# Performance work log

Measured on AMD Instinct MI355X. Metric: run time of the kernel, lower is better.

## Reference

```python
import jax, jax.numpy as jnp
import numpy as np

FORGET_BIAS = 1.0

def _lstm_step(c, h, x, W, b):
    # TF BasicLSTMCell: concat([x, h]) @ W + b -> split into i, j, f, o
    gates = jnp.concatenate([x, h], axis=-1) @ W + b
    i, j, f, o = jnp.split(gates, 4, axis=-1)
    new_c = c * jax.nn.sigmoid(f + FORGET_BIAS) + jax.nn.sigmoid(i) * jnp.tanh(j)
    new_h = jnp.tanh(new_c) * jax.nn.sigmoid(o)
    return new_c, new_h

def setup_inputs() -> dict:
    key = jax.random.key(0)
    ks = jax.random.split(key, 8)
    B, T, D, H, C = 64, 128, 2048, 512, 101
    s1 = 1.0 / np.sqrt(D + H)
    s2 = 1.0 / np.sqrt(2 * H)
    so = 1.0 / np.sqrt(H)
    return {
        "inputs": jax.random.normal(ks[0], (B, T, D), dtype=jnp.float32),
        "labels": jax.random.randint(ks[1], (B, T), 0, C, dtype=jnp.int64),
        "W1": jax.random.normal(ks[2], (D + H, 4 * H), dtype=jnp.float32) * s1,
        "b1": jnp.zeros((4 * H,), dtype=jnp.float32),
        "W2": jax.random.normal(ks[3], (2 * H, 4 * H), dtype=jnp.float32) * s2,
        "b2": jnp.zeros((4 * H,), dtype=jnp.float32),
        "Wout": jax.random.normal(ks[4], (H, C), dtype=jnp.float32) * so,
        "bout": jnp.zeros((C,), dtype=jnp.float32),
    }

def reference(inputs, labels, W1, b1, W2, b2, Wout, bout):
    B, T, D = inputs.shape
    H = Wout.shape[0]

    def step(carry, x_t):
        (c1, h1), (c2, h2) = carry
        c1, h1 = _lstm_step(c1, h1, x_t, W1, b1)
        c2, h2 = _lstm_step(c2, h2, h1, W2, b2)
        return ((c1, h1), (c2, h2)), h2

    zeros = jnp.zeros((B, H), dtype=inputs.dtype)
    init = ((zeros, zeros), (zeros, zeros))
    xs = jnp.swapaxes(inputs, 0, 1)  # [T, B, D]
    _, hs = jax.lax.scan(step, init, xs)  # hs: [T, B, H]
    outputs = jnp.swapaxes(hs, 0, 1)  # [B, T, H]

    logits = outputs @ Wout + bout  # [B, T, C]
    preds = jax.nn.softmax(logits, axis=-1)
    log_probs = jax.nn.log_softmax(logits, axis=-1)
    ce = -jnp.take_along_axis(log_probs, labels[..., None], axis=-1)[..., 0]  # [B, T]
    cost = jnp.mean(jnp.sum(ce, axis=1))
    return preds, cost
```

## Files before the change

### kernel.cpp

```cpp
#include <hip/hip_runtime.h>
#include <cmath>

#define Bb   64
#define Tt   128
#define Dd   2048
#define Hh   512
#define Gg   2048
#define Cc   101
#define PC   112
#define ROWS 8192

typedef unsigned short u16;
typedef __attribute__((ext_vector_type(8))) short bf16x8;
typedef __attribute__((ext_vector_type(4))) float f32x4;

#define PAD32 40
#define PAD128 136

#define GLOAD_LDS16(g, l) __builtin_amdgcn_global_load_lds(                  \
    (const __attribute__((address_space(1))) unsigned int*)(const void*)(g), \
    (__attribute__((address_space(3))) unsigned int*)(void*)(l), 16, 0, 0)

__device__ __forceinline__ u16 bf16rne(float x) {
  unsigned u = __float_as_uint(x);
  unsigned r = (u + 0x7fffu + ((u >> 16) & 1u)) >> 16;
  return (u16)r;
}
__device__ __forceinline__ void split_bf16(float x, u16& h, u16& l) {
  h = bf16rne(x);
  l = bf16rne(x - __uint_as_float(((unsigned)h) << 16));
}
__device__ __forceinline__ float sigm(float x) { return 1.f / (1.f + expf(-x)); }

__global__ __launch_bounds__(256)
void convert_hilo(const float* __restrict__ src, u16* __restrict__ hi,
                  u16* __restrict__ lo, int n4) {
  for (int i = blockIdx.x * 256 + threadIdx.x; i < n4; i += gridDim.x * 256) {
    const float4 v = ((const float4*)src)[i];
    ushort4 h, l;
    split_bf16(v.x, h.x, l.x);
    split_bf16(v.y, h.y, l.y);
    split_bf16(v.z, h.z, l.z);
    split_bf16(v.w, h.w, l.w);
    ((ushort4*)hi)[i] = h;
    ((ushort4*)lo)[i] = l;
  }
}

__global__ __launch_bounds__(256)
void convertT_w1(const float* __restrict__ W1, u16* __restrict__ Th,
                 u16* __restrict__ Tl) {
  __shared__ float tl[32][33];
  const int tx = threadIdx.x, ty = threadIdx.y;
  const int k0 = blockIdx.x * 32, c0 = blockIdx.y * 32;
#pragma unroll
  for (int j = 0; j < 4; ++j)
    tl[ty + j * 8][tx] = W1[(size_t)(k0 + ty + j * 8) * Gg + (c0 + tx)];
  __syncthreads();
#pragma unroll
  for (int j = 0; j < 4; ++j) {
    const float v = tl[tx][ty + j * 8];
    u16 h, l;
    split_bf16(v, h, l);
    const size_t o = (size_t)(c0 + ty + j * 8) * Dd + (k0 + tx);
    Th[o] = h;
    Tl[o] = l;
  }
}

__global__ __launch_bounds__(256)
void convert_woutT(const float* __restrict__ Wout, u16* __restrict__ Th,
                   u16* __restrict__ Tl) {
  const int c = blockIdx.x;
  for (int k = threadIdx.x; k < Hh; k += 256) {
    const float v = (c < Cc) ? Wout[k * Cc + c] : 0.f;
    u16 h, l;
    split_bf16(v, h, l);
    Th[c * Hh + k] = h;
    Tl[c * Hh + k] = l;
  }
}

__global__ __launch_bounds__(256)
void permuteW(const float* __restrict__ src, u16* __restrict__ dh,
              u16* __restrict__ dl, int K) {
  __shared__ float tl[32][33];
  const int tx = threadIdx.x, ty = threadIdx.y;
  const int k0 = blockIdx.x * 32, c0 = blockIdx.y * 32;
#pragma unroll
  for (int j = 0; j < 4; ++j)
    tl[ty + j * 8][tx] = src[(size_t)(k0 + ty + j * 8) * Gg + (c0 + tx)];
  __syncthreads();
#pragma unroll
  for (int j = 0; j < 4; ++j) {
    const int col = c0 + ty + j * 8;
    const int g = col >> 9, mg = col & 511;
    const int cg = mg >> 2, m = mg & 3;
    const float v = tl[tx][ty + j * 8];
    u16 h, l;
    split_bf16(v, h, l);
    const size_t o = (size_t)(cg * 16 + g * 4 + m) * K + k0 + tx;
    dh[o] = h;
    dl[o] = l;
  }
}

__global__ __launch_bounds__(256)
void gemm1_mfma(const u16* __restrict__ Ah, const u16* __restrict__ Al,
                const u16* __restrict__ Bh, const u16* __restrict__ Bl,
                const float* __restrict__ bias, float* __restrict__ C) {
  __shared__ u16 Ash[128][32];
  __shared__ u16 Asl[128][32];
  __shared__ u16 Bsh[128][32];
  __shared__ u16 Bsl[128][32];
  const int tid  = threadIdx.x;
  const int lane = tid & 63, wave = tid >> 6;
  const int wm = wave >> 1, wn = wave & 1;
  const int l15 = lane & 15, q = lane >> 4, r4 = (lane >> 4) * 4;
  const int lin = blockIdx.x;
  const int xcd = lin & 7, s = lin >> 3;
  const int bx = 2 * xcd + (s & 1);
  const int by = s >> 1;
  const int row0 = by * 128, col0 = bx * 128;

  const int sr = tid >> 2, sc = (tid & 3) * 8;
  const u16* gA0h = Ah + (size_t)(row0 + sr) * Dd + sc;
  const u16* gA1h = Ah + (size_t)(row0 + 64 + sr) * Dd + sc;
  const u16* gA0l = Al + (size_t)(row0 + sr) * Dd + sc;
  const u16* gA1l = Al + (size_t)(row0 + 64 + sr) * Dd + sc;
  const u16* gB0h = Bh + (size_t)(col0 + sr) * Dd + sc;
  const u16* gB1h = Bh + (size_t)(col0 + 64 + sr) * Dd + sc;
  const u16* gB0l = Bl + (size_t)(col0 + sr) * Dd + sc;
  const u16* gB1l = Bl + (size_t)(col0 + 64 + sr) * Dd + sc;
  u16* lA0h = &Ash[sr][sc];      u16* lA1h = &Ash[64 + sr][sc];
  u16* lA0l = &Asl[sr][sc];      u16* lA1l = &Asl[64 + sr][sc];
  u16* lB0h = &Bsh[sr][sc];      u16* lB1h = &Bsh[64 + sr][sc];
  u16* lB0l = &Bsl[sr][sc];      u16* lB1l = &Bsl[64 + sr][sc];

  f32x4 acc[4][4];
#pragma unroll
  for (int i = 0; i < 4; ++i)
#pragma unroll
    for (int j = 0; j < 4; ++j) acc[i][j] = (f32x4){0.f, 0.f, 0.f, 0.f};

  for (int k0 = 0; k0 < Dd; k0 += 32) {
    GLOAD_LDS16(gA0h + k0, lA0h);
    GLOAD_LDS16(gA1h + k0, lA1h);
    GLOAD_LDS16(gA0l + k0, lA0l);
    GLOAD_LDS16(gA1l + k0, lA1l);
    GLOAD_LDS16(gB0h + k0, lB0h);
    GLOAD_LDS16(gB1h + k0, lB1h);
    GLOAD_LDS16(gB0l + k0, lB0l);
    GLOAD_LDS16(gB1l + k0, lB1l);
    __syncthreads();

    bf16x8 afh[4], afl[4], bfh[4], bfl[4];
#pragma unroll
    for (int mt = 0; mt < 4; ++mt) {
      const int row = wm * 64 + mt * 16 + l15;
      afh[mt] = *(const bf16x8*)(&Ash[row][q * 8]);
      afl[mt] = *(const bf16x8*)(&Asl[row][q * 8]);
    }
#pragma unroll
    for (int nt = 0; nt < 4; ++nt) {
      const int row = wn * 64 + nt * 16 + l15;
      bfh[nt] = *(const bf16x8*)(&Bsh[row][q * 8]);
      bfl[nt] = *(const bf16x8*)(&Bsl[row][q * 8]);
    }
#pragma unroll
    for (int mt = 0; mt < 4; ++mt)
#pragma unroll
      for (int nt = 0; nt < 4; ++nt) {
        acc[mt][nt] = __builtin_amdgcn_mfma_f32_16x16x32_bf16(
            afh[mt], bfh[nt], acc[mt][nt], 0, 0, 0);
        acc[mt][nt] = __builtin_amdgcn_mfma_f32_16x16x32_bf16(
            afh[mt], bfl[nt], acc[mt][nt], 0, 0, 0);
        acc[mt][nt] = __builtin_amdgcn_mfma_f32_16x16x32_bf16(
            afl[mt], bfh[nt], acc[mt][nt], 0, 0, 0);
      }
    __syncthreads();
  }

#pragma unroll
  for (int nt = 0; nt < 4; ++nt) {
    const int col = col0 + wn * 64 + nt * 16 + l15;
    const float bj = bias[col];
#pragma unroll
    for (int mt = 0; mt < 4; ++mt) {
      float* Cp = C + (size_t)(row0 + wm * 64 + mt * 16 + r4) * Gg + col;
#pragma unroll
      for (int r = 0; r < 4; ++r)
        Cp[(size_t)r * Gg] = acc[mt][nt][r] + bj;
    }
  }
}

__global__ __launch_bounds__(256)
void gemm_proj(const u16* __restrict__ Ah, const u16* __restrict__ Al,
               const u16* __restrict__ Bh, const u16* __restrict__ Bl,
               const float* __restrict__ bout, const int* __restrict__ labels,
               float* __restrict__ preds, float* __restrict__ ce) {
  __shared__ u16 Ash[128][PAD32];
  __shared__ u16 Asl[128][PAD32];
  __shared__ u16 Bsh[PC][PAD32];
  __shared__ u16 Bsl[PC][PAD32];
  const int tid  = threadIdx.x;
  const int lane = tid & 63, wave = tid >> 6;
  const int l15 = lane & 15, k8 = (lane >> 4) * 8, r4 = (lane >> 4) * 4;
  const int row0 = blockIdx.x * 128;
  const int srow = tid >> 1, sk = (tid & 1) * 16;

  const u16* pAh = Ah + (size_t)(row0 + srow) * Hh + sk;
  const u16* pAl = Al + (size_t)(row0 + srow) * Hh + sk;
  const u16* pBh = Bh + (size_t)srow * Hh + sk;
  const u16* pBl = Bl + (size_t)srow * Hh + sk;

  f32x4 acc[2][7];
#pragma unroll
  for (int i = 0; i < 2; ++i)
#pragma unroll
    for (int j = 0; j < 7; ++j) acc[i][j] = (f32x4){0.f, 0.f, 0.f, 0.f};

  for (int k0 = 0; k0 < Hh; k0 += 32) {
    *(bf16x8*)(&Ash[srow][sk])     = *(const bf16x8*)(pAh + k0);
    *(bf16x8*)(&Ash[srow][sk + 8]) = *(const bf16x8*)(pAh + k0 + 8);
    *(bf16x8*)(&Asl[srow][sk])     = *(const bf16x8*)(pAl + k0);
    *(bf16x8*)(&Asl[srow][sk + 8]) = *(const bf16x8*)(pAl + k0 + 8);
    if (srow < PC) {
      *(bf16x8*)(&Bsh[srow][sk])     = *(const bf16x8*)(pBh + k0);
      *(bf16x8*)(&Bsh[srow][sk + 8]) = *(const bf16x8*)(pBh + k0 + 8);
      *(bf16x8*)(&Bsl[srow][sk])     = *(const bf16x8*)(pBl + k0);
      *(bf16x8*)(&Bsl[srow][sk + 8]) = *(const bf16x8*)(pBl + k0 + 8);
    }
    __syncthreads();

    bf16x8 afh[2], afl[2], bfh[7], bfl[7];
#pragma unroll
    for (int mt = 0; mt < 2; ++mt) {
      afh[mt] = *(const bf16x8*)(&Ash[wave * 32 + mt * 16 + l15][k8]);
      afl[mt] = *(const bf16x8*)(&Asl[wave * 32 + mt * 16 + l15][k8]);
    }
#pragma unroll
    for (int nt = 0; nt < 7; ++nt) {
      bfh[nt] = *(const bf16x8*)(&Bsh[nt * 16 + l15][k8]);
      bfl[nt] = *(const bf16x8*)(&Bsl[nt * 16 + l15][k8]);
    }
#pragma unroll
    for (int mt = 0; mt < 2; ++mt)
#pragma unroll
      for (int nt = 0; nt < 7; ++nt) {
        acc[mt][nt] = __builtin_amdgcn_mfma_f32_16x16x32_bf16(
            afh[mt], bfh[nt], acc[mt][nt], 0, 0, 0);
        acc[mt][nt] = __builtin_amdgcn_mfma_f32_16x16x32_bf16(
            afh[mt], bfl[nt], acc[mt][nt], 0, 0, 0);
        acc[mt][nt] = __builtin_amdgcn_mfma_f32_16x16x32_bf16(
            afl[mt], bfh[nt], acc[mt][nt], 0, 0, 0);
      }
    __syncthreads();
  }

  float bj[7];
#pragma unroll
  for (int nt = 0; nt < 7; ++nt) {
    const int col = nt * 16 + l15;
    bj[nt] = (col < Cc) ? bout[col] : 0.f;
  }

#pragma unroll
  for (int mt = 0; mt < 2; ++mt)
#pragma unroll
    for (int r = 0; r < 4; ++r) {
      const int row = row0 + wave * 32 + mt * 16 + r4 + r;
      float v[7];
      float mx = -INFINITY;
#pragma unroll
      for (int nt = 0; nt < 7; ++nt) {
        const int col = nt * 16 + l15;
        v[nt] = acc[mt][nt][r] + bj[nt];
        if (col < Cc) mx = fmaxf(mx, v[nt]);
      }
#pragma unroll
      for (int off = 1; off < 16; off <<= 1) mx = fmaxf(mx, __shfl_xor(mx, off));
      float e[7];
      float sum = 0.f;
#pragma unroll
      for (int nt = 0; nt < 7; ++nt) {
        const int col = nt * 16 + l15;
        e[nt] = (col < Cc) ? expf(v[nt] - mx) : 0.f;
        sum += e[nt];
      }
#pragma unroll
      for (int off = 1; off < 16; off <<= 1) sum += __shfl_xor(sum, off);
      const float inv = 1.f / sum;
#pragma unroll
      for (int nt = 0; nt < 7; ++nt) {
        const int col = nt * 16 + l15;
        if (col < Cc) preds[(size_t)row * Cc + col] = e[nt] * inv;
      }
      const int lab = labels[row];
#pragma unroll
      for (int nt = 0; nt < 7; ++nt) {
        if (nt * 16 + l15 == lab)
          ce[row] = logf(sum) + mx - v[nt];
      }
    }
}

#define BM 128
#define BN 128
#define BK 16

__global__ __launch_bounds__(256)
void sgemm_bias(const float* __restrict__ A, const float* __restrict__ B,
                const float* __restrict__ bias, float* __restrict__ C,
                int M, int N, int K) {
  __shared__ float As[BK][BM];
  __shared__ float Bs[BK][BN];
  const int tid  = threadIdx.x;
  const int row0 = blockIdx.y * BM, col0 = blockIdx.x * BN;
  const int tr = (tid >> 4) << 3;
  const int tc = (tid & 15) << 3;

  float acc[8][8];
#pragma unroll
  for (int i = 0; i < 8; ++i)
#pragma unroll
    for (int j = 0; j < 8; ++j) acc[i][j] = 0.f;

  const int arow = tid >> 1;
  const int acol = (tid & 1) << 3;
  const int brow = tid >> 4;
  const int bcol = (tid & 15) << 3;
  const float* Ap = A + (size_t)(row0 + arow) * K + acol;
  const float* Bp = B + (size_t)brow * N + (col0 + bcol);

  for (int k0 = 0; k0 < K; k0 += BK) {
    const float4 a0 = *(const float4*)(Ap + k0);
    const float4 a1 = *(const float4*)(Ap + k0 + 4);
    const float4 bv0 = *(const float4*)(Bp + (size_t)k0 * N);
    const float4 bv1 = *(const float4*)(Bp + (size_t)k0 * N + 4);
    As[acol + 0][arow] = a0.x;
    As[acol + 1][arow] = a0.y;
    As[acol + 2][arow] = a0.z;
    As[acol + 3][arow] = a0.w;
    As[acol + 4][arow] = a1.x;
    As[acol + 5][arow] = a1.y;
    As[acol + 6][arow] = a1.z;
    As[acol + 7][arow] = a1.w;
    *(float4*)(&Bs[brow][bcol])     = bv0;
    *(float4*)(&Bs[brow][bcol + 4]) = bv1;
    __syncthreads();
#pragma unroll
    for (int k = 0; k < BK; ++k) {
      float a[8], b[8];
      *(float4*)(a)     = *(const float4*)(&As[k][tr]);
      *(float4*)(a + 4) = *(const float4*)(&As[k][tr + 4]);
      *(float4*)(b)     = *(const float4*)(&Bs[k][tc]);
      *(float4*)(b + 4) = *(const float4*)(&Bs[k][tc + 4]);
#pragma unroll
      for (int i = 0; i < 8; ++i)
#pragma unroll
        for (int j = 0; j < 8; ++j)
          acc[i][j] = fmaf(a[i], b[j], acc[i][j]);
    }
    __syncthreads();
  }

  float bj[8];
#pragma unroll
  for (int j = 0; j < 8; ++j) bj[j] = bias[col0 + tc + j];
#pragma unroll
  for (int i = 0; i < 8; ++i) {
    float* Cp = C + (size_t)(row0 + tr + i) * N + (col0 + tc);
    float4 o0, o1;
    o0.x = acc[i][0] + bj[0]; o0.y = acc[i][1] + bj[1];
    o0.z = acc[i][2] + bj[2]; o0.w = acc[i][3] + bj[3];
    o1.x = acc[i][4] + bj[4]; o1.y = acc[i][5] + bj[5];
    o1.z = acc[i][6] + bj[6]; o1.w = acc[i][7] + bj[7];
    *(float4*)(Cp)     = o0;
    *(float4*)(Cp + 4) = o1;
  }
}

__global__ __launch_bounds__(256, 4)
void fused_step4(const float* __restrict__ pre,
                 const u16* __restrict__ WP1h, const u16* __restrict__ WP1l,
                 const u16* __restrict__ WP2h, const u16* __restrict__ WP2l,
                 const float* __restrict__ b2,
                 u16* __restrict__ h1hi, u16* __restrict__ h1lo,
                 u16* __restrict__ h2hi, u16* __restrict__ h2lo,
                 u16* __restrict__ h2fh, u16* __restrict__ h2fl,
                 float* __restrict__ c1, float* __restrict__ c2, int t) {
  __shared__ u16 Ah[2][16][PAD128], Al[2][16][PAD128];
  __shared__ u16 Bh[2][16][PAD128], Bl[2][16][PAD128];
  __shared__ float ex[4][16][17];
  const int tid = threadIdx.x;
  const int lane = tid & 63, kh = tid >> 6;
  const int fr = lane & 15, f8 = (lane >> 4) * 8, r4 = (lane >> 4) * 4;
  const bool isL2 = blockIdx.x >= 512;
  const int idx = blockIdx.x & 511;
  const int cg = idx & 127, bg = idx >> 7;
  const int b0 = bg * 16;

  const int hr = tid >> 4, hk = (tid & 15) * 8;

  f32x4 acc = {0.f, 0.f, 0.f, 0.f};
  bool have = false;
  float p0 = 0.f, p1 = 0.f, p2 = 0.f, p3 = 0.f;

  const int eb = tid >> 2, em = tid & 3;
  const int col = cg * 4 + em;
  const int ci = (b0 + eb) * Hh + col;

  if (!isL2) {
    if (t >= Tt) return;
    if (tid < 64) {
      const float* pp = pre + ((size_t)(b0 + eb) * Tt + t) * Gg + col;
      p0 = pp[0]; p1 = pp[512]; p2 = pp[1024]; p3 = pp[1536];
    }
    if (t > 0) {
      const int sl = (t - 1) & 1;
      const u16* A_h = h1hi + (sl << 15) + (b0 + hr) * 512 + hk;
      const u16* A_l = h1lo + (sl << 15) + (b0 + hr) * 512 + hk;
      const u16* B_h = WP1h + (size_t)(cg * 16 + hr) * 512 + hk;
      const u16* B_l = WP1l + (size_t)(cg * 16 + hr) * 512 + hk;

      bf16x8 ra, rl_, rbh, rbl;
      ra = *(const bf16x8*)(A_h);   rl_ = *(const bf16x8*)(A_l);
      rbh = *(const bf16x8*)(B_h);  rbl = *(const bf16x8*)(B_l);
      *(bf16x8*)&Ah[0][hr][hk] = ra;   *(bf16x8*)&Al[0][hr][hk] = rl_;
      *(bf16x8*)&Bh[0][hr][hk] = rbh;  *(bf16x8*)&Bl[0][hr][hk] = rbl;
      __syncthreads();

      for (int kc = 0; kc < 4; ++kc) {
        const int cur = kc & 1;
        if (kc < 3) {
          const int ko = (kc + 1) * 128;
          ra = *(const bf16x8*)(A_h + ko);   rl_ = *(const bf16x8*)(A_l + ko);
          rbh = *(const bf16x8*)(B_h + ko);  rbl = *(const bf16x8*)(B_l + ko);
        }
        {
          const int c0 = kh * 32 + f8;
          const bf16x8 afh = *(const bf16x8*)&Ah[cur][fr][c0];
          const bf16x8 afl = *(const bf16x8*)&Al[cur][fr][c0];
          const bf16x8 bfh = *(const bf16x8*)&Bh[cur][fr][c0];
          const bf16x8 bfl = *(const bf16x8*)&Bl[cur][fr][c0];
          acc = __builtin_amdgcn_mfma_f32_16x16x32_bf16(afh, bfh, acc, 0, 0, 0);
          acc = __builtin_amdgcn_mfma_f32_16x16x32_bf16(afh, bfl, acc, 0, 0, 0);
          acc = __builtin_amdgcn_mfma_f32_16x16x32_bf16(afl, bfh, acc, 0, 0, 0);
        }
        if (kc < 3) {
          const int nb = cur ^ 1;
          *(bf16x8*)&Ah[nb][hr][hk] = ra;   *(bf16x8*)&Al[nb][hr][hk] = rl_;
          *(bf16x8*)&Bh[nb][hr][hk] = rbh;  *(bf16x8*)&Bl[nb][hr][hk] = rbl;
        }
        __syncthreads();
      }
      have = true;
    }
  } else {
    if (t < 1) return;
    const u16* A1h = h1hi + (((t - 1) & 1) << 15) + (b0 + hr) * 512 + hk;
    const u16* A1l = h1lo + (((t - 1) & 1) << 15) + (b0 + hr) * 512 + hk;
    const u16* A2h = h2hi + (((t - 2) & 1) << 15) + (b0 + hr) * 512 + hk;
    const u16* A2l = h2lo + (((t - 2) & 1) << 15) + (b0 + hr) * 512 + hk;
    const u16* B_h = WP2h + (size_t)(cg * 16 + hr) * 1024 + hk;
    const u16* B_l = WP2l + (size_t)(cg * 16 + hr) * 1024 + hk;
    const bool h2ok = (t >= 2);

    bf16x8 ra, rl_, rbh, rbl;
    ra = *(const bf16x8*)(A1h);   rl_ = *(const bf16x8*)(A1l);
    rbh = *(const bf16x8*)(B_h);  rbl = *(const bf16x8*)(B_l);
    *(bf16x8*)&Ah[0][hr][hk] = ra;   *(bf16x8*)&Al[0][hr][hk] = rl_;
    *(bf16x8*)&Bh[0][hr][hk] = rbh;  *(bf16x8*)&Bl[0][hr][hk] = rbl;
    __syncthreads();

    for (int kc = 0; kc < 8; ++kc) {
      const int cur = kc & 1;
      if (kc < 7) {
        const int nk = kc + 1;
        const u16* sh  = (nk < 4) ? A1h : A2h;
        const u16* sl2 = (nk < 4) ? A1l : A2l;
        const int ko = (nk & 3) * 128;
        ra = *(const bf16x8*)(sh + ko);    rl_ = *(const bf16x8*)(sl2 + ko);
        rbh = *(const bf16x8*)(B_h + nk * 128);
        rbl = *(const bf16x8*)(B_l + nk * 128);
      }
      if (kc < 4 || h2ok) {
        const int c0 = kh * 32 + f8;
        const bf16x8 afh = *(const bf16x8*)&Ah[cur][fr][c0];
        const bf16x8 afl = *(const bf16x8*)&Al[cur][fr][c0];
        const bf16x8 bfh = *(const bf16x8*)&Bh[cur][fr][c0];
        const bf16x8 bfl = *(const bf16x8*)&Bl[cur][fr][c0];
        acc = __builtin_amdgcn_mfma_f32_16x16x32_bf16(afh, bfh, acc, 0, 0, 0);
        acc = __builtin_amdgcn_mfma_f32_16x16x32_bf16(afh, bfl, acc, 0, 0, 0);
        acc = __builtin_amdgcn_mfma_f32_16x16x32_bf16(afl, bfh, acc, 0, 0, 0);
      }
      if (kc < 7) {
        const int nb = cur ^ 1;
        *(bf16x8*)&Ah[nb][hr][hk] = ra;   *(bf16x8*)&Al[nb][hr][hk] = rl_;
        *(bf16x8*)&Bh[nb][hr][hk] = rbh;  *(bf16x8*)&Bl[nb][hr][hk] = rbl;
      }
      __syncthreads();
    }
    have = true;
  }

  if (have) {
#pragma unroll
    for (int r = 0; r < 4; ++r)
      ex[kh][r4 + r][fr] = acc[r];
  }
  __syncthreads();

  if (tid < 64) {
    float s0 = 0.f, s1 = 0.f, s2 = 0.f, s3 = 0.f;
    if (have) {
#pragma unroll
      for (int q = 0; q < 4; ++q) {
        s0 += ex[q][eb][0 + em];
        s1 += ex[q][eb][4 + em];
        s2 += ex[q][eb][8 + em];
        s3 += ex[q][eb][12 + em];
      }
    }
    if (!isL2) {
      const float gi = p0 + s0, gj = p1 + s1, gf = p2 + s2, go = p3 + s3;
      const float cp = (t > 0) ? c1[ci] : 0.f;
      const float nc = fmaf(cp, sigm(gf + 1.f), sigm(gi) * tanhf(gj));
      c1[ci] = nc;
      const float nh = tanhf(nc) * sigm(go);
      u16 hh, hl;
      split_bf16(nh, hh, hl);
      const int hidx = ((t & 1) << 15) + ci;
      h1hi[hidx] = hh;
      h1lo[hidx] = hl;
    } else {
      const float gi = b2[col] + s0, gj = b2[512 + col] + s1;
      const float gf = b2[1024 + col] + s2, go = b2[1536 + col] + s3;
      const float cp = (t >= 2) ? c2[ci] : 0.f;
      const float nc = fmaf(cp, sigm(gf + 1.f), sigm(gi) * tanhf(gj));
      c2[ci] = nc;
      const float nh = tanhf(nc) * sigm(go);
      u16 hh, hl;
      split_bf16(nh, hh, hl);
      const int hidx = (((t - 1) & 1) << 15) + ci;
      h2hi[hidx] = hh;
      h2lo[hidx] = hl;
      const size_t fo = ((size_t)(b0 + eb) * Tt + (t - 1)) * Hh + col;
      h2fh[fo] = hh;
      h2fl[fo] = hl;
    }
  }
}

__global__ __launch_bounds__(256)
void reduce_cost(const float* __restrict__ ce, float* __restrict__ out) {
  __shared__ float red[256];
  const int tid = threadIdx.x;
  float s = 0.f;
  for (int i = tid; i < ROWS; i += 256) s += ce[i];
  red[tid] = s;
  __syncthreads();
  for (int st = 128; st > 0; st >>= 1) {
    if (tid < st) red[tid] += red[tid + st];
    __syncthreads();
  }
  if (tid == 0) out[0] = red[0] / (float)Bb;
}

extern "C" void kernel_launch(void* const* d_in, const int* in_sizes, int n_in,
                              void* d_out, int out_size, void* d_ws, size_t ws_size,
                              hipStream_t stream) {
  const float* inputs = (const float*)d_in[0];
  const int*   labels = (const int*)d_in[1];
  const float* W1     = (const float*)d_in[2];
  const float* b1     = (const float*)d_in[3];
  const float* W2     = (const float*)d_in[4];
  const float* b2     = (const float*)d_in[5];
  const float* Wout   = (const float*)d_in[6];
  const float* bout   = (const float*)d_in[7];
  float* out = (float*)d_out;

  float* ws     = (float*)d_ws;
  float* pre    = ws;
  float* c1     = pre    + (size_t)ROWS * Gg;
  float* c2     = c1     + (size_t)Bb * Hh;
  float* ceb    = c2     + (size_t)Bb * Hh;
  u16* h1hi = (u16*)(ceb + ROWS);
  u16* h1lo = h1hi + 2 * 64 * 512;
  u16* h2hi = h1lo + 2 * 64 * 512;
  u16* h2lo = h2hi + 2 * 64 * 512;
  u16* h2fh = h2lo + 2 * 64 * 512;
  u16* h2fl = h2fh + (size_t)ROWS * Hh;
  u16* WP1h = h2fl + (size_t)ROWS * Hh;
  u16* WP1l = WP1h + 128 * 16 * 512;
  u16* WP2h = WP1l + 128 * 16 * 512;
  u16* WP2l = WP2h + 128 * 16 * 1024;
  u16* WoTh = WP2l + 128 * 16 * 1024;
  u16* WoTl = WoTh + PC * Hh;
  u16* Xhi  = WoTl + PC * Hh;
  u16* Xlo  = Xhi  + (size_t)ROWS * Dd;
  u16* W1Th = Xlo  + (size_t)ROWS * Dd;
  u16* W1Tl = W1Th + (size_t)Gg * Dd;
  const size_t need = (size_t)((char*)(W1Tl + (size_t)Gg * Dd) - (char*)d_ws);
  const bool use_mfma = ws_size >= need;

  permuteW<<<dim3(16, 64), dim3(32, 8), 0, stream>>>(
      W1 + (size_t)Dd * Gg, WP1h, WP1l, 512);
  permuteW<<<dim3(32, 64), dim3(32, 8), 0, stream>>>(W2, WP2h, WP2l, 1024);
  convert_woutT<<<PC, 256, 0, stream>>>(Wout, WoTh, WoTl);

  if (use_mfma) {
    convert_hilo<<<2048, 256, 0, stream>>>(inputs, Xhi, Xlo, ROWS * Dd / 4);
    convertT_w1<<<dim3(64, 64), dim3(32, 8), 0, stream>>>(W1, W1Th, W1Tl);
    gemm1_mfma<<<1024, 256, 0, stream>>>(Xhi, Xlo, W1Th, W1Tl, b1, pre);
  } else {
    sgemm_bias<<<dim3(Gg / BN, ROWS / BM), dim3(256), 0, stream>>>(
        inputs, W1, b1, pre, ROWS, Gg, Dd);
  }

  for (int t = 0; t <= Tt; ++t)
    fused_step4<<<1024, 256, 0, stream>>>(pre, WP1h, WP1l, WP2h, WP2l, b2,
                                          h1hi, h1lo, h2hi, h2lo,
                                          h2fh, h2fl, c1, c2, t);

  gemm_proj<<<ROWS / 128, 256, 0, stream>>>(h2fh, h2fl, WoTh, WoTl, bout,
                                            labels, out, ceb);
  reduce_cost<<<1, 256, 0, stream>>>(ceb, out + (size_t)ROWS * Cc);
}
```

Measured before the change: 1.481 ms.

## Stage full K slab via direct global-to-LDS loads with XOR swizzle in recurrent step

After: 1.484 ms. No clear change (+0.2%).

```diff
diff --git a/kernel.cpp b/kernel.cpp
--- a/kernel.cpp
+++ b/kernel.cpp
@@ -15,7 +15,6 @@
 typedef __attribute__((ext_vector_type(4))) float f32x4;
 
 #define PAD32 40
-#define PAD128 136
 
 #define GLOAD_LDS16(g, l) __builtin_amdgcn_global_load_lds(                  \
     (const __attribute__((address_space(1))) unsigned int*)(const void*)(g), \
@@ -382,8 +381,8 @@
   }
 }
 
-__global__ __launch_bounds__(256, 4)
-void fused_step4(const float* __restrict__ pre,
+__global__ __launch_bounds__(256, 2)
+void fused_step5(const float* __restrict__ pre,
                  const u16* __restrict__ WP1h, const u16* __restrict__ WP1l,
                  const u16* __restrict__ WP2h, const u16* __restrict__ WP2l,
                  const float* __restrict__ b2,
@@ -391,18 +390,20 @@
                  u16* __restrict__ h2hi, u16* __restrict__ h2lo,
                  u16* __restrict__ h2fh, u16* __restrict__ h2fl,
                  float* __restrict__ c1, float* __restrict__ c2, int t) {
-  __shared__ u16 Ah[2][16][PAD128], Al[2][16][PAD128];
-  __shared__ u16 Bh[2][16][PAD128], Bl[2][16][PAD128];
+  __shared__ u16 Ash[16][512], Asl[16][512];
+  __shared__ u16 Bsh[16][512], Bsl[16][512];
   __shared__ float ex[4][16][17];
   const int tid = threadIdx.x;
   const int lane = tid & 63, kh = tid >> 6;
-  const int fr = lane & 15, f8 = (lane >> 4) * 8, r4 = (lane >> 4) * 4;
+  const int fr = lane & 15, q = lane >> 4, r4 = (lane >> 4) * 4;
   const bool isL2 = blockIdx.x >= 512;
   const int idx = blockIdx.x & 511;
   const int cg = idx & 127, bg = idx >> 7;
   const int b0 = bg * 16;
 
-  const int hr = tid >> 4, hk = (tid & 15) * 8;
+  const int strow[4] = {0 * 4 + (tid >> 6), 1 * 4 + (tid >> 6),
+                        2 * 4 + (tid >> 6), 3 * 4 + (tid >> 6)};
+  const int lslot = tid & 63;
 
   f32x4 acc = {0.f, 0.f, 0.f, 0.f};
   bool have = false;
@@ -411,6 +412,33 @@
   const int eb = tid >> 2, em = tid & 3;
   const int col = cg * 4 + em;
   const int ci = (b0 + eb) * Hh + col;
+
+#define STAGE4(gbase, RS, lds)                                             \
+  {                                                                        \
+    _Pragma("unroll")                                                      \
+    for (int p = 0; p < 4; ++p) {                                          \
+      const int row = strow[p];                                            \
+      const int gs = lslot ^ (row & 7);                                    \
+      GLOAD_LDS16((gbase) + (size_t)row * (RS) + gs * 8,                   \
+                  &(lds)[row][lslot * 8]);                                 \
+    }                                                                      \
+  }
+
+#define COMPUTE4()                                                         \
+  {                                                                        \
+    _Pragma("unroll")                                                      \
+    for (int s = 0; s < 4; ++s) {                                          \
+      const int slot = kh * 16 + s * 4 + q;                                \
+      const int rs = (slot ^ (fr & 7)) * 8;                                \
+      const bf16x8 afh = *(const bf16x8*)&Ash[fr][rs];                     \
+      const bf16x8 afl = *(const bf16x8*)&Asl[fr][rs];                     \
+      const bf16x8 bfh = *(const bf16x8*)&Bsh[fr][rs];                     \
+      const bf16x8 bfl = *(const bf16x8*)&Bsl[fr][rs];                     \
+      acc = __builtin_amdgcn_mfma_f32_16x16x32_bf16(afh, bfh, acc, 0, 0, 0);\
+      acc = __builtin_amdgcn_mfma_f32_16x16x32_bf16(afh, bfl, acc, 0, 0, 0);\
+      acc = __builtin_amdgcn_mfma_f32_16x16x32_bf16(afl, bfh, acc, 0, 0, 0);\
+    }                                                                      \
+  }
 
   if (!isL2) {
     if (t >= Tt) return;
@@ -420,91 +448,41 @@
     }
     if (t > 0) {
       const int sl = (t - 1) & 1;
-      const u16* A_h = h1hi + (sl << 15) + (b0 + hr) * 512 + hk;
-      const u16* A_l = h1lo + (sl << 15) + (b0 + hr) * 512 + hk;
-      const u16* B_h = WP1h + (size_t)(cg * 16 + hr) * 512 + hk;
-      const u16* B_l = WP1l + (size_t)(cg * 16 + hr) * 512 + hk;
-
-      bf16x8 ra, rl_, rbh, rbl;
-      ra = *(const bf16x8*)(A_h);   rl_ = *(const bf16x8*)(A_l);
-      rbh = *(const bf16x8*)(B_h);  rbl = *(const bf16x8*)(B_l);
-      *(bf16x8*)&Ah[0][hr][hk] = ra;   *(bf16x8*)&Al[0][hr][hk] = rl_;
-      *(bf16x8*)&Bh[0][hr][hk] = rbh;  *(bf16x8*)&Bl[0][hr][hk] = rbl;
+      STAGE4(h1hi + (sl << 15) + b0 * 512, 512, Ash);
+      STAGE4(h1lo + (sl << 15) + b0 * 512, 512, Asl);
+      STAGE4(WP1h + (size_t)cg * 16 * 512, 512, Bsh);
+      STAGE4(WP1l + (size_t)cg * 16 * 512, 512, Bsl);
       __syncthreads();
-
-      for (int kc = 0; kc < 4; ++kc) {
-        const int cur = kc & 1;
-        if (kc < 3) {
-          const int ko = (kc + 1) * 128;
-          ra = *(const bf16x8*)(A_h + ko);   rl_ = *(const bf16x8*)(A_l + ko);
-          rbh = *(const bf16x8*)(B_h + ko);  rbl = *(const bf16x8*)(B_l + ko);
-        }
-        {
-          const int c0 = kh * 32 + f8;
-          const bf16x8 afh = *(const bf16x8*)&Ah[cur][fr][c0];
-          const bf16x8 afl = *(const bf16x8*)&Al[cur][fr][c0];
-          const bf16x8 bfh = *(const bf16x8*)&Bh[cur][fr][c0];
-          const bf16x8 bfl = *(const bf16x8*)&Bl[cur][fr][c0];
-          acc = __builtin_amdgcn_mfma_f32_16x16x32_bf16(afh, bfh, acc, 0, 0, 0);
-          acc = __builtin_amdgcn_mfma_f32_16x16x32_bf16(afh, bfl, acc, 0, 0, 0);
-          acc = __builtin_amdgcn_mfma_f32_16x16x32_bf16(afl, bfh, acc, 0, 0, 0);
-        }
-        if (kc < 3) {
-          const int nb = cur ^ 1;
-          *(bf16x8*)&Ah[nb][hr][hk] = ra;   *(bf16x8*)&Al[nb][hr][hk] = rl_;
-          *(bf16x8*)&Bh[nb][hr][hk] = rbh;  *(bf16x8*)&Bl[nb][hr][hk] = rbl;
-        }
-        __syncthreads();
-      }
+      COMPUTE4();
       have = true;
     }
   } else {
     if (t < 1) return;
-    const u16* A1h = h1hi + (((t - 1) & 1) << 15) + (b0 + hr) * 512 + hk;
-    const u16* A1l = h1lo + (((t - 1) & 1) << 15) + (b0 + hr) * 512 + hk;
-    const u16* A2h = h2hi + (((t - 2) & 1) << 15) + (b0 + hr) * 512 + hk;
-    const u16* A2l = h2lo + (((t - 2) & 1) << 15) + (b0 + hr) * 512 + hk;
-    const u16* B_h = WP2h + (size_t)(cg * 16 + hr) * 1024 + hk;
-    const u16* B_l = WP2l + (size_t)(cg * 16 + hr) * 1024 + hk;
-    const bool h2ok = (t >= 2);
-
-    bf16x8 ra, rl_, rbh, rbl;
-    ra = *(const bf16x8*)(A1h);   rl_ = *(const bf16x8*)(A1l);
-    rbh = *(const bf16x8*)(B_h);  rbl = *(const bf16x8*)(B_l);
-    *(bf16x8*)&Ah[0][hr][hk] = ra;   *(bf16x8*)&Al[0][hr][hk] = rl_;
-    *(bf16x8*)&Bh[0][hr][hk] = rbh;  *(bf16x8*)&Bl[0][hr][hk] = rbl;
-    __syncthreads();
-
-    for (int kc = 0; kc < 8; ++kc) {
-      const int cur = kc & 1;
-      if (kc < 7) {
-        const int nk = kc + 1;
-        const u16* sh  = (nk < 4) ? A1h : A2h;
-        const u16* sl2 = (nk < 4) ? A1l : A2l;
-        const int ko = (nk & 3) * 128;
-        ra = *(const bf16x8*)(sh + ko);    rl_ = *(const bf16x8*)(sl2 + ko);
-        rbh = *(const bf16x8*)(B_h + nk * 128);
-        rbl = *(const bf16x8*)(B_l + nk * 128);
-      }
-      if (kc < 4 || h2ok) {
-        const int c0 = kh * 32 + f8;
-        const bf16x8 afh = *(const bf16x8*)&Ah[cur][fr][c0];
-        const bf16x8 afl = *(const bf16x8*)&Al[cur][fr][c0];
-        const bf16x8 bfh = *(const bf16x8*)&Bh[cur][fr][c0];
-        const bf16x8 bfl = *(const bf16x8*)&Bl[cur][fr][c0];
-        acc = __builtin_amdgcn_mfma_f32_16x16x32_bf16(afh, bfh, acc, 0, 0, 0);
-        acc = __builtin_amdgcn_mfma_f32_16x16x32_bf16(afh, bfl, acc, 0, 0, 0);
-        acc = __builtin_amdgcn_mfma_f32_16x16x32_bf16(afl, bfh, acc, 0, 0, 0);
-      }
-      if (kc < 7) {
-        const int nb = cur ^ 1;
-        *(bf16x8*)&Ah[nb][hr][hk] = ra;   *(bf16x8*)&Al[nb][hr][hk] = rl_;
-        *(bf16x8*)&Bh[nb][hr][hk] = rbh;  *(bf16x8*)&Bl[nb][hr][hk] = rbl;
-      }
+    const u16* Wbh = WP2h + (size_t)cg * 16 * 1024;
+    const u16* Wbl = WP2l + (size_t)cg * 16 * 1024;
+    {
+      const int sl = (t - 1) & 1;
+      STAGE4(h1hi + (sl << 15) + b0 * 512, 512, Ash);
+      STAGE4(h1lo + (sl << 15) + b0 * 512, 512, Asl);
+      STAGE4(Wbh, 1024, Bsh);
+      STAGE4(Wbl, 1024, Bsl);
       __syncthreads();
+      COMPUTE4();
+    }
+    if (t >= 2) {
+      __syncthreads();
+      const int sl = (t - 2) & 1;
+      STAGE4(h2hi + (sl << 15) + b0 * 512, 512, Ash);
+      STAGE4(h2lo + (sl << 15) + b0 * 512, 512, Asl);
+      STAGE4(Wbh + 512, 1024, Bsh);
+      STAGE4(Wbl + 512, 1024, Bsl);
+      __syncthreads();
+      COMPUTE4();
     }
     have = true;
   }
+#undef STAGE4
+#undef COMPUTE4
 
   if (have) {
 #pragma unroll
@@ -517,11 +495,11 @@
     float s0 = 0.f, s1 = 0.f, s2 = 0.f, s3 = 0.f;
     if (have) {
 #pragma unroll
-      for (int q = 0; q < 4; ++q) {
-        s0 += ex[q][eb][0 + em];
-        s1 += ex[q][eb][4 + em];
-        s2 += ex[q][eb][8 + em];
-        s3 += ex[q][eb][12 + em];
+      for (int w = 0; w < 4; ++w) {
+        s0 += ex[w][eb][0 + em];
+        s1 += ex[w][eb][4 + em];
+        s2 += ex[w][eb][8 + em];
+        s3 += ex[w][eb][12 + em];
       }
     }
     if (!isL2) {
@@ -621,7 +599,7 @@
   }
 
   for (int t = 0; t <= Tt; ++t)
-    fused_step4<<<1024, 256, 0, stream>>>(pre, WP1h, WP1l, WP2h, WP2l, b2,
+    fused_step5<<<1024, 256, 0, stream>>>(pre, WP1h, WP1l, WP2h, WP2l, b2,
                                           h1hi, h1lo, h2hi, h2lo,
                                           h2fh, h2fl, c1, c2, t);
 
```
